# Performance work log

Hardware: AMD Instinct MI355X
Metric: run time of the kernel (lower is better)

The kernel has to match this reference:

```python
import jax, jax.numpy as jnp
import numpy as np
from jax import lax

EPS = 1e-8

def _norm(v, eps=EPS):
    # matches torch F.normalize: v / max(||v||, eps)
    return v / jnp.maximum(jnp.linalg.norm(v, axis=-1, keepdims=True), eps)

def keep_r6(r6):
    v1 = _norm(r6[..., :3])
    v2 = r6[..., 3:6]
    v2 = v2 - jnp.sum(v2 * v1, axis=-1, keepdims=True) * v1
    v2n = jnp.linalg.norm(v2, axis=-1, keepdims=True)
    mask = (v2n < 1e-6).astype(r6.dtype)
    e1 = jnp.array([1.0, 0.0, 0.0], dtype=r6.dtype)
    e2 = jnp.array([0.0, 1.0, 0.0], dtype=r6.dtype)
    dot = jnp.abs(jnp.sum(v1 * e1, axis=-1, keepdims=True))
    fb = jnp.where(dot < 0.9, e1, e2)
    fb_v2 = jnp.cross(v1, jnp.broadcast_to(fb, v1.shape), axis=-1)
    v2 = (1.0 - mask) * v2 + mask * fb_v2
    v2 = _norm(v2)
    return jnp.concatenate([v1, v2], axis=-1)

def r6_to_matrix(r6):
    r6 = keep_r6(r6)
    v1, v2 = r6[..., :3], r6[..., 3:6]
    v3 = jnp.cross(v1, v2, axis=-1)
    R = jnp.stack([v1, v2, v3], axis=-1)  # columns v1,v2,v3
    det = jnp.linalg.det(R)
    return R * jnp.sign(det)[..., None, None]

def instance_norm(x, eps=1e-5):
    # InstanceNorm3d, affine=False: per-(B,C) stats over spatial dims, biased var
    mu = jnp.mean(x, axis=(2, 3, 4), keepdims=True)
    var = jnp.mean((x - mu) ** 2, axis=(2, 3, 4), keepdims=True)
    return (x - mu) * lax.rsqrt(var + eps)

def conv1x1(x, w, b):
    return jnp.einsum('oc,bcdhw->bodhw', w[:, :, 0, 0, 0], x) + b[None, :, None, None, None]

def conv3_circ(x, w, b):
    xp = jnp.pad(x, ((0, 0), (0, 0), (1, 1), (1, 1), (1, 1)), mode='wrap')
    out = lax.conv_general_dilated(xp, w, (1, 1, 1), 'VALID',
                                   dimension_numbers=('NCDHW', 'OIDHW', 'NCDHW'))
    return out + b[None, :, None, None, None]

def _gelu(t):
    return jax.nn.gelu(t, approximate=False)

def _forward(x, pos_emb, qkv_w, qkv_b, lp1_w, lp1_b, lp2_w, lp2_b,
             mod1_w, mod1_b, mod2_w, mod2_b, pa_w, pa_b,
             R6_d, R6_h, R6_w, proj_w, proj_b):
    B, C, D, H, W = x.shape
    NH = pa_w.shape[0]
    HD = C // NH
    NV = HD // 3
    scale = HD ** (-0.5)

    # PositionalProcessing (deterministic; computed once, reused for all 3 axes)
    local = conv1x1(_gelu(instance_norm(conv3_circ(pos_emb, lp1_w, lp1_b))), lp2_w, lp2_b)
    mod = jax.nn.sigmoid(conv1x1(_gelu(instance_norm(conv1x1(local, mod1_w, mod1_b))), mod2_w, mod2_b))
    x_mod = x * mod
    pos_attn = _gelu(instance_norm(conv1x1(pos_emb, pa_w, pa_b)))  # [B,NH,D,H,W]

    axes = [
        (R6_d, (0, 3, 4, 1, 2), (0, 4, 3, 1, 2)),  # depth
        (R6_h, (0, 2, 4, 1, 3), (0, 4, 1, 3, 2)),  # height
        (R6_w, (0, 2, 3, 1, 4), (0, 4, 1, 2, 3)),  # width
    ]
    out_sum = 0.0
    for R6, perm, inv in axes:
        xp = jnp.transpose(x_mod, perm)      # [B, A1, A2, C, L]
        Bb, A1, A2, _, L = xp.shape
        bd = Bb * A1 * A2
        xl = jnp.swapaxes(xp.reshape(bd, C, L), -1, -2)  # [bd, L, C]
        qkv = (xl @ qkv_w.T + qkv_b).reshape(bd, L, 3, NH, HD)
        qkv = jnp.transpose(qkv, (2, 0, 3, 1, 4))
        q, k, v = qkv[0], qkv[1], qkv[2]     # [bd, NH, L, HD]
        R = r6_to_matrix(keep_r6(R6))[0]     # [NH, 3, 3]

        def rot(t):
            tv = t.reshape(bd, NH, L, NV, 3)
            return jnp.einsum('hij,bhlvj->bhlvi', R, tv).reshape(bd, NH, L, HD)

        attn = jnp.einsum('bhqd,bhkd->bhqk', rot(q), rot(k)) * scale
        pa = jnp.transpose(pos_attn, perm).reshape(bd, NH, L)
        attn = jax.nn.softmax(attn + pa[..., None], axis=-1)
        o = jnp.einsum('bhqk,bhkd->bhqd', attn, v)      # [bd, NH, L, HD]
        o = jnp.swapaxes(o, 1, 2).reshape(Bb, A1, A2, L, C)
        out_sum = out_sum + jnp.transpose(o, inv)        # [B, C, D, H, W]
    return conv1x1(out_sum, proj_w, proj_b)


def setup_inputs() -> dict:
    key = jax.random.key(0)
    ks = jax.random.split(key, 20)
    B, C, D, H, W, NH = 2, 96, 40, 40, 40, 4

    def rn(k, shape, s=0.05):
        return jax.random.normal(k, shape, dtype=jnp.float32) * s

    return {
        'x': jax.random.normal(ks[0], (B, C, D, H, W), dtype=jnp.float32),
        'pos_emb': jax.random.normal(ks[1], (B, C, D, H, W), dtype=jnp.float32),
        'qkv_w': rn(ks[2], (3 * C, C)), 'qkv_b': rn(ks[3], (3 * C,)),
        'lp1_w': rn(ks[4], (C, C, 3, 3, 3)), 'lp1_b': rn(ks[5], (C,)),
        'lp2_w': rn(ks[6], (C, C, 1, 1, 1)), 'lp2_b': rn(ks[7], (C,)),
        'mod1_w': rn(ks[8], (C, C, 1, 1, 1)), 'mod1_b': rn(ks[9], (C,)),
        'mod2_w': rn(ks[10], (C, C, 1, 1, 1)), 'mod2_b': rn(ks[11], (C,)),
        'pa_w': rn(ks[12], (NH, C, 1, 1, 1)), 'pa_b': rn(ks[13], (NH,)),
        'R6_d': jax.random.normal(ks[14], (1, NH, 6), dtype=jnp.float32),
        'R6_h': jax.random.normal(ks[15], (1, NH, 6), dtype=jnp.float32),
        'R6_w': jax.random.normal(ks[16], (1, NH, 6), dtype=jnp.float32),
        'proj_w': rn(ks[17], (C, C, 1, 1, 1)), 'proj_b': rn(ks[18], (C,)),
    }


def reference(x, pos_emb, qkv_w, qkv_b, lp1_w, lp1_b, lp2_w, lp2_b,
              mod1_w, mod1_b, mod2_w, mod2_b, pa_w, pa_b,
              R6_d, R6_h, R6_w, proj_w, proj_b):
    return _forward(x, pos_emb, qkv_w, qkv_b, lp1_w, lp1_b, lp2_w, lp2_b,
                    mod1_w, mod1_b, mod2_w, mod2_b, pa_w, pa_b,
                    R6_d, R6_h, R6_w, proj_w, proj_b)
```

## Files before the change

### kernel.cpp

```cpp
#include <hip/hip_runtime.h>


typedef __attribute__((ext_vector_type(8))) _Float16 half8;
typedef __attribute__((ext_vector_type(2))) _Float16 half2;
typedef __attribute__((ext_vector_type(16))) float floatx16;

static __device__ __forceinline__ half2 h2(unsigned int u) {
    return __builtin_bit_cast(half2, u);
}
static __device__ __forceinline__ float fdot2(unsigned int a, unsigned int b, float c) {
    return __builtin_amdgcn_fdot2(h2(a), h2(b), c, false);
}

__global__ void k_zero(float* __restrict__ p) {
    int t = threadIdx.x;
    for (int i = t; i < 768; i += 256) p[i] = 0.f;
}

__global__ __launch_bounds__(256) void k_cvt_in(const float* __restrict__ pos,
                                                _Float16* __restrict__ in_t) {
    __shared__ _Float16 lds[64][97];
    int bid = blockIdx.x;
    int b = bid / 1000, s0 = (bid % 1000) * 64;
    int t = threadIdx.x;
    for (int i = t; i < 6144; i += 256) {
        int c = i / 64, sl = i % 64;
        lds[sl][c] = (_Float16)pos[(b * 96 + c) * 64000 + s0 + sl];
    }
    __syncthreads();
    _Float16* outp = in_t + ((size_t)b * 64000 + s0) * 96;
    for (int i = t; i < 6144; i += 256) {
        int sl = i / 96, c = i % 96;
        outp[i] = lds[sl][c];
    }
}

__global__ void k_cvt_w(const float* __restrict__ w, _Float16* __restrict__ wf) {
    int i = blockIdx.x * 256 + threadIdx.x;
    if (i < 248832) {
        int c = i % 96, m = (i / 96) % 96, tap = i / 9216;
        wf[i] = (_Float16)w[(m * 96 + c) * 27 + tap];
    }
}

__global__ void k_cvt_f16(const float* __restrict__ w, _Float16* __restrict__ o, int n) {
    int i = blockIdx.x * 256 + threadIdx.x;
    if (i < n) o[i] = (_Float16)w[i];
}

__global__ __launch_bounds__(256) void k_fold(const float* __restrict__ lp2_w,
                                              const float* __restrict__ lp2_b,
                                              const float* __restrict__ mod1_w,
                                              const float* __restrict__ mod1_b,
                                              _Float16* __restrict__ wfold,
                                              float* __restrict__ bfold) {
    int i = blockIdx.x * 256 + threadIdx.x;
    if (i < 9216) {
        int o = i / 96, c = i % 96;
        float a = 0.f;
        for (int k = 0; k < 96; k++) a += mod1_w[o * 96 + k] * lp2_w[k * 96 + c];
        wfold[i] = (_Float16)a;
    }
    if (blockIdx.x == 0 && threadIdx.x < 96) {
        int o = threadIdx.x;
        float a = mod1_b[o];
        for (int k = 0; k < 96; k++) a += mod1_w[o * 96 + k] * lp2_b[k];
        bfold[o] = a;
    }
}

__global__ __launch_bounds__(256) void k_conv3_v2(const _Float16* __restrict__ in_t,
                                                  const _Float16* __restrict__ wf,
                                                  const float* __restrict__ bias,
                                                  _Float16* __restrict__ c3) {
    __shared__ int tbl[27 * 256];
    __shared__ _Float16 st[256 * 98];
    __shared__ float bsh[96];
    int t = threadIdx.x;
    int bid = blockIdx.x;
    int b = bid / 250;
    int s0 = (bid % 250) * 256;

    for (int u = t; u < 27 * 256; u += 256) {
        int tap = u >> 8, nl = u & 255;
        int kd = tap / 9, kh = (tap / 3) % 3, kw = tap % 3;
        int s = s0 + nl;
        int d = s / 1600, r = s - d * 1600;
        int h = r / 40, w = r - h * 40;
        int ds = d + kd - 1; if (ds < 0) ds += 40; else if (ds >= 40) ds -= 40;
        int hs = h + kh - 1; if (hs < 0) hs += 40; else if (hs >= 40) hs -= 40;
        int wv2 = w + kw - 1; if (wv2 < 0) wv2 += 40; else if (wv2 >= 40) wv2 -= 40;
        tbl[u] = ((ds * 1600 + hs * 40 + wv2) * 96) * 2;
    }
    if (t < 96) bsh[t] = bias[t];
    __syncthreads();

    int wv = t >> 6, lane = t & 63;
    int n31 = lane & 31, kg = lane >> 5;
    const char* inb = (const char*)(in_t + (size_t)b * 64000 * 96) + kg * 16;

    floatx16 acc[3][2];
#pragma unroll
    for (int mt = 0; mt < 3; mt++)
#pragma unroll
        for (int nt = 0; nt < 2; nt++)
#pragma unroll
            for (int r = 0; r < 16; r++) acc[mt][nt][r] = 0.f;

    for (int tap = 0; tap < 27; tap++) {
        int ta0 = tbl[tap * 256 + wv * 64 + n31];
        int ta1 = tbl[tap * 256 + wv * 64 + 32 + n31];
        const char* pb0 = inb + ta0;
        const char* pb1 = inb + ta1;
        const _Float16* wt = wf + tap * 9216 + kg * 8;
#pragma unroll
        for (int j = 0; j < 6; j++) {
            half8 a0 = *(const half8*)(wt + (n31) * 96 + j * 16);
            half8 a1 = *(const half8*)(wt + (32 + n31) * 96 + j * 16);
            half8 a2 = *(const half8*)(wt + (64 + n31) * 96 + j * 16);
            half8 b0 = *(const half8*)(pb0 + j * 32);
            half8 b1 = *(const half8*)(pb1 + j * 32);
            acc[0][0] = __builtin_amdgcn_mfma_f32_32x32x16_f16(a0, b0, acc[0][0], 0, 0, 0);
            acc[0][1] = __builtin_amdgcn_mfma_f32_32x32x16_f16(a0, b1, acc[0][1], 0, 0, 0);
            acc[1][0] = __builtin_amdgcn_mfma_f32_32x32x16_f16(a1, b0, acc[1][0], 0, 0, 0);
            acc[1][1] = __builtin_amdgcn_mfma_f32_32x32x16_f16(a1, b1, acc[1][1], 0, 0, 0);
            acc[2][0] = __builtin_amdgcn_mfma_f32_32x32x16_f16(a2, b0, acc[2][0], 0, 0, 0);
            acc[2][1] = __builtin_amdgcn_mfma_f32_32x32x16_f16(a2, b1, acc[2][1], 0, 0, 0);
        }
    }

#pragma unroll
    for (int mt = 0; mt < 3; mt++)
#pragma unroll
        for (int nt = 0; nt < 2; nt++)
#pragma unroll
            for (int r = 0; r < 16; r++) {
                int m = mt * 32 + (r & 3) + 8 * (r >> 2) + 4 * kg;
                int sl = wv * 64 + nt * 32 + n31;
                st[sl * 98 + m] = (_Float16)(acc[mt][nt][r] + bsh[m]);
            }
    __syncthreads();

    unsigned int* dst = (unsigned int*)(c3 + ((size_t)(b * 64000 + s0)) * 96);
    for (int i = t; i < 12288; i += 256) {
        int row = i / 48, sg = i % 48;
        dst[i] = *(const unsigned int*)&st[row * 98 + sg * 2];
    }
}

__global__ __launch_bounds__(192) void k_stats_sc(const _Float16* __restrict__ in,
                                                  float* __restrict__ raw) {
    __shared__ float red_s[16][96], red_q[16][96];
    int bid = blockIdx.x;
    int b = bid / 50, ch = bid % 50;
    int t = threadIdx.x;
    int sp = t / 12, cs = t % 12;
    const uint4* base = (const uint4*)(in + ((size_t)(b * 64000 + ch * 1280)) * 96);
    float s8[8], q8[8];
#pragma unroll
    for (int e = 0; e < 8; e++) { s8[e] = 0.f; q8[e] = 0.f; }
    for (int i = 0; i < 80; i++) {
        uint4 v = base[(sp + i * 16) * 12 + cs];
        half8 h = __builtin_bit_cast(half8, v);
#pragma unroll
        for (int e = 0; e < 8; e++) { float f = (float)h[e]; s8[e] += f; q8[e] += f * f; }
    }
#pragma unroll
    for (int e = 0; e < 8; e++) { red_s[sp][cs * 8 + e] = s8[e]; red_q[sp][cs * 8 + e] = q8[e]; }
    __syncthreads();
    if (t < 96) {
        float S = 0.f, Q = 0.f;
        for (int k = 0; k < 16; k++) { S += red_s[k][t]; Q += red_q[k][t]; }
        atomicAdd(&raw[(b * 96 + t) * 2], S);
        atomicAdd(&raw[(b * 96 + t) * 2 + 1], Q);
    }
}

__global__ void k_finalize(const float* __restrict__ raw, float2* __restrict__ sf) {
    int t = threadIdx.x;
    if (t < 192) {
        float S = raw[t * 2], Q = raw[t * 2 + 1];
        float mu = S * (1.f / 64000.f);
        float var = Q * (1.f / 64000.f) - mu * mu;
        sf[t] = make_float2(mu, rsqrtf(var + 1e-5f));
    }
}

__global__ __launch_bounds__(256) void k_ng16(_Float16* __restrict__ x, const float2* __restrict__ sf) {
    int t = threadIdx.x, bid = blockIdx.x;
    uint4* p = (uint4*)x;
#pragma unroll
    for (int k = 0; k < 4; k++) {
        int i = bid * 1024 + k * 256 + t;
        int e0 = i * 8;
        int b = e0 / 6144000;
        int c0 = e0 % 96;
        const float2* sp = &sf[b * 96 + c0];
        uint4 v = p[i];
        half8 h = __builtin_bit_cast(half8, v);
        _Float16 o[8];
#pragma unroll
        for (int e = 0; e < 8; e++) {
            float2 st = sp[e];
            float u = ((float)h[e] - st.x) * st.y;
            o[e] = (_Float16)(0.5f * u * (1.f + erff(u * 0.70710678118654752f)));
        }
        p[i] = *(uint4*)o;
    }
}

template <int MODE>
__global__ __launch_bounds__(256) void k_gemm96(const _Float16* __restrict__ in,
                                                const _Float16* __restrict__ w,
                                                const float* __restrict__ bias,
                                                const float* __restrict__ xg,
                                                _Float16* __restrict__ outp) {
    __shared__ _Float16 un[12544];
    __shared__ float bias_s[96];
    int t = threadIdx.x, bid = blockIdx.x;
    int b = bid / 500, s0 = (bid % 500) * 128;
    for (int i = t; i < 1152; i += 256) ((uint4*)un)[i] = ((const uint4*)w)[i];
    if (t < 96) bias_s[t] = bias[t];
    __syncthreads();

    int ws = t >> 6, lane = t & 63;
    int n = lane & 31, kg = lane >> 5;
    int p = ws * 32 + n;
    const uint4* brow = (const uint4*)(in + ((size_t)(b * 64000 + s0 + p)) * 96);
    uint4 bf[6];
#pragma unroll
    for (int kc = 0; kc < 6; kc++) bf[kc] = brow[kc * 2 + kg];

    floatx16 acc[3];
#pragma unroll
    for (int mt = 0; mt < 3; mt++)
#pragma unroll
        for (int r = 0; r < 16; r++) acc[mt][r] = 0.f;
#pragma unroll
    for (int kc = 0; kc < 6; kc++) {
        half8 bfh = __builtin_bit_cast(half8, bf[kc]);
#pragma unroll
        for (int mt = 0; mt < 3; mt++) {
            uint4 au = *(const uint4*)&un[(mt * 32 + n) * 96 + kc * 16 + kg * 8];
            acc[mt] = __builtin_amdgcn_mfma_f32_32x32x16_f16(__builtin_bit_cast(half8, au), bfh, acc[mt], 0, 0, 0);
        }
    }
    __syncthreads();

#pragma unroll
    for (int mt = 0; mt < 3; mt++)
#pragma unroll
        for (int r = 0; r < 16; r++) {
            int m = mt * 32 + (r & 3) + 8 * (r >> 2) + 4 * kg;
            int sl = ws * 32 + n;
            float v = acc[mt][r] + bias_s[m];
            if (MODE == 1) {
                v = 1.f / (1.f + __expf(-v));
                v *= xg[((size_t)(b * 96 + m)) * 64000 + s0 + sl];
            }
            un[sl * 98 + m] = (_Float16)v;
        }
    __syncthreads();

    unsigned int* dst = (unsigned int*)(outp + ((size_t)(b * 64000 + s0)) * 96);
    for (int i = t; i < 6144; i += 256) {
        int row = i / 48, sg = i % 48;
        dst[i] = *(const unsigned int*)&un[row * 98 + sg * 2];
    }
}

__global__ __launch_bounds__(256) void k_qkv(const _Float16* __restrict__ xt,
                                             const _Float16* __restrict__ wq,
                                             const float* __restrict__ qb,
                                             _Float16* __restrict__ qA) {
    __shared__ _Float16 smem[27648];
    __shared__ float bias_s[288];
    int t = threadIdx.x;
    int bid = blockIdx.x;
    int b = bid / 500;
    int s0 = (bid % 500) * 128;

    for (int i = t; i < 3456; i += 256) ((uint4*)smem)[i] = ((const uint4*)wq)[i];
    for (int i = t; i < 288; i += 256) bias_s[i] = qb[i];
    __syncthreads();

    int ws = t >> 6, lane = t & 63;
    int n = lane & 31, kg = lane >> 5;
    int p = ws * 32 + n;

    const uint4* brow = (const uint4*)(xt + ((size_t)(b * 64000 + s0 + p)) * 96);
    uint4 bf[6];
#pragma unroll
    for (int kc = 0; kc < 6; kc++) bf[kc] = brow[kc * 2 + kg];

    floatx16 acc[9];
#pragma unroll
    for (int mt = 0; mt < 9; mt++)
#pragma unroll
        for (int r = 0; r < 16; r++) acc[mt][r] = 0.f;

#pragma unroll
    for (int kc = 0; kc < 6; kc++) {
        half8 bfh = __builtin_bit_cast(half8, bf[kc]);
#pragma unroll
        for (int mt = 0; mt < 9; mt++) {
            uint4 au = *(const uint4*)&smem[(mt * 32 + n) * 96 + kc * 16 + kg * 8];
            acc[mt] = __builtin_amdgcn_mfma_f32_32x32x16_f16(__builtin_bit_cast(half8, au), bfh, acc[mt], 0, 0, 0);
        }
    }

    const float scale = 0.20412414523193154f;
    for (int q = 0; q < 2; q++) {
        __syncthreads();
        if ((ws >> 1) == q) {
            int pl = (ws & 1) * 32 + n;
#pragma unroll
            for (int mt = 0; mt < 9; mt++)
#pragma unroll
                for (int g = 0; g < 4; g++) {
                    int m0 = mt * 32 + g * 8 + kg * 4;
                    _Float16 tm[4];
#pragma unroll
                    for (int j = 0; j < 4; j++) {
                        float v = acc[mt][g * 4 + j] + bias_s[m0 + j];
                        if (m0 + j < 96) v *= scale;
                        tm[j] = (_Float16)v;
                    }
                    *(uint2*)&smem[pl * 296 + m0] = *(uint2*)tm;
                }
        }
        __syncthreads();
        for (int idx = t; idx < 2304; idx += 256) {
            int pl = idx / 36, seg = idx % 36;
            int s = s0 + q * 64 + pl;
            uint4 v = *(const uint4*)&smem[pl * 296 + seg * 8];
            *(uint4*)&qA[((size_t)(b * 64000 + s)) * 288 + seg * 8] = v;
        }
    }
}

template <int AXIS, bool ACC>
__global__ __launch_bounds__(320, 3) void k_attn(const _Float16* __restrict__ qA,
                                                 _Float16* __restrict__ osum) {
    __shared__ _Float16 kk[8352];
    __shared__ _Float16 vT[7744];
    int t = threadIdx.x;
    int bid = blockIdx.x;
    int b = bid / 800;
    int r0 = (bid % 800) * 2;

    auto smap = [&](int r, int l) -> int {
        if (AXIS == 0) return l * 1600 + r;
        else if (AXIS == 1) { int d = r / 40, w = r % 40; return d * 1600 + l * 40 + w; }
        else return r * 40 + l;
    };
    const uint4* src = (const uint4*)qA;
    for (int i = t; i < 960; i += 320) {
        int line = i / 480, key = (i % 480) / 12, seg = i % 12;
        int row = b * 64000 + smap(r0 + line, key);
        ((uint4*)kk)[i] = src[(size_t)row * 36 + 12 + seg];
    }
    for (int i = t; i < 960; i += 320) {
        int line = i / 480, key = (i % 480) / 12, seg = i % 12;
        int row = b * 64000 + smap(r0 + line, key);
        uint4 v = src[(size_t)row * 36 + 24 + seg];
        _Float16 tmp[8];
        *(uint4*)tmp = v;
#pragma unroll
        for (int e = 0; e < 8; e++) {
            int hdg = seg * 8 + e;
            vT[(line * 4 + hdg / 24) * 968 + (hdg % 24) * 40 + key] = tmp[e];
        }
    }

    int line = t / 160, head = (t % 160) / 40, ql = t % 40;
    int rr = r0 + line;
    unsigned int qu[12];
    {
        const uint4* qp = (const uint4*)(qA + ((size_t)(b * 64000 + smap(rr, ql))) * 288 + head * 24);
#pragma unroll
        for (int j = 0; j < 3; j++) *(uint4*)&qu[j * 4] = qp[j];
    }
    __syncthreads();

    float s[40];
    const uint4* kbase = (const uint4*)kk + line * 480 + head * 3;
#pragma unroll 4
    for (int key = 0; key < 40; key++) {
        unsigned int kku[12];
#pragma unroll
        for (int j = 0; j < 3; j++) *(uint4*)&kku[j * 4] = kbase[key * 12 + j];
        float a = 0.f;
#pragma unroll
        for (int i = 0; i < 12; i++) a = fdot2(kku[i], qu[i], a);
        s[key] = a;
    }

    float mx = -1e30f;
#pragma unroll
    for (int i = 0; i < 40; i++) mx = fmaxf(mx, s[i]);
    float sum = 0.f;
#pragma unroll
    for (int i = 0; i < 40; i++) { s[i] = __expf(s[i] - mx); sum += s[i]; }
    float inv = 1.f / sum;

    unsigned int pw[20];
#pragma unroll
    for (int i = 0; i < 20; i++) {
        half2 a = { (_Float16)(s[2 * i] * inv), (_Float16)(s[2 * i + 1] * inv) };
        pw[i] = __builtin_bit_cast(unsigned int, a);
    }

    __syncthreads();

    float o[24];
    const uint4* vbase = (const uint4*)vT + (line * 4 + head) * 121;
#pragma unroll 2
    for (int hd = 0; hd < 24; hd++) {
        unsigned int vv[20];
#pragma unroll
        for (int j = 0; j < 5; j++) *(uint4*)&vv[j * 4] = vbase[hd * 5 + j];
        float a = 0.f;
#pragma unroll
        for (int i = 0; i < 20; i++) a = fdot2(vv[i], pw[i], a);
        o[hd] = a;
    }

    {
        _Float16 tm[24];
#pragma unroll
        for (int j = 0; j < 24; j++) tm[j] = (_Float16)o[j];
        _Float16* dA = &kk[(line * 40 + ql) * 104 + head * 24];
#pragma unroll
        for (int j = 0; j < 3; j++) ((uint4*)dA)[j] = ((uint4*)tm)[j];
    }
    __syncthreads();

    uint4* dst = (uint4*)osum;
    for (int i = t; i < 960; i += 320) {
        int row = i / 12, seg = i % 12;
        int s2 = smap(r0 + row / 40, row % 40);
        size_t di = ((size_t)(b * 64000 + s2)) * 12 + seg;
        uint4 v = *(const uint4*)&kk[row * 104 + seg * 8];
        if (ACC) {
            half8 a = __builtin_bit_cast(half8, dst[di]);
            half8 c = __builtin_bit_cast(half8, v);
            dst[di] = __builtin_bit_cast(uint4, a + c);
        } else {
            dst[di] = v;
        }
    }
}

__global__ __launch_bounds__(256) void k_proj(const _Float16* __restrict__ osum,
                                              const _Float16* __restrict__ wp,
                                              const float* __restrict__ pb,
                                              float* __restrict__ out) {
    __shared__ _Float16 A[9216];
    __shared__ float bias_s[96];
    int t = threadIdx.x;
    int bid = blockIdx.x;
    int b = bid / 500;
    int s0 = (bid % 500) * 128;
    for (int i = t; i < 1152; i += 256) ((uint4*)A)[i] = ((const uint4*)wp)[i];
    if (t < 96) bias_s[t] = pb[t];
    __syncthreads();

    int ws = t >> 6, lane = t & 63;
    int n = lane & 31, kg = lane >> 5;
    int s = s0 + ws * 32 + n;

    const uint4* brow = (const uint4*)(osum + ((size_t)(b * 64000 + s0 + ws * 32 + n)) * 96);
    uint4 bf[6];
#pragma unroll
    for (int kc = 0; kc < 6; kc++) bf[kc] = brow[kc * 2 + kg];

    floatx16 acc[3];
#pragma unroll
    for (int mt = 0; mt < 3; mt++)
#pragma unroll
        for (int r = 0; r < 16; r++) acc[mt][r] = 0.f;

#pragma unroll
    for (int kc = 0; kc < 6; kc++) {
        half8 bfh = __builtin_bit_cast(half8, bf[kc]);
#pragma unroll
        for (int mt = 0; mt < 3; mt++) {
            uint4 au = *(const uint4*)&A[(mt * 32 + n) * 96 + kc * 16 + kg * 8];
            acc[mt] = __builtin_amdgcn_mfma_f32_32x32x16_f16(__builtin_bit_cast(half8, au), bfh, acc[mt], 0, 0, 0);
        }
    }

#pragma unroll
    for (int mt = 0; mt < 3; mt++)
#pragma unroll
        for (int r = 0; r < 16; r++) {
            int m = mt * 32 + (r & 3) + 8 * (r >> 2) + 4 * kg;
            out[((size_t)(b * 96 + m)) * 64000 + s] = acc[mt][r] + bias_s[m];
        }
}

extern "C" void kernel_launch(void* const* d_in, const int* in_sizes, int n_in,
                              void* d_out, int out_size, void* d_ws, size_t ws_size,
                              hipStream_t stream) {
    const float* x      = (const float*)d_in[0];
    const float* pos    = (const float*)d_in[1];
    const float* qkv_w  = (const float*)d_in[2];
    const float* qkv_b  = (const float*)d_in[3];
    const float* lp1_w  = (const float*)d_in[4];
    const float* lp1_b  = (const float*)d_in[5];
    const float* lp2_w  = (const float*)d_in[6];
    const float* lp2_b  = (const float*)d_in[7];
    const float* mod1_w = (const float*)d_in[8];
    const float* mod1_b = (const float*)d_in[9];
    const float* mod2_w = (const float*)d_in[10];
    const float* mod2_b = (const float*)d_in[11];
    const float* proj_w = (const float*)d_in[17];
    const float* proj_b = (const float*)d_in[18];
    float* out = (float*)d_out;
    float* ws = (float*)d_ws;

    _Float16* bufA = (_Float16*)ws;
    _Float16* bufB = (_Float16*)(ws + 6144000);
    _Float16* qA   = (_Float16*)(ws + 12288000);
    _Float16* in_t = qA;
    _Float16* wf   = (_Float16*)(ws + 30720000);
    _Float16* wq   = (_Float16*)(ws + 30844416);
    _Float16* wpj  = (_Float16*)(ws + 30858240);
    _Float16* wfold= (_Float16*)(ws + 30862848);
    _Float16* wm2  = (_Float16*)(ws + 30867456);
    float* bfold   = ws + 30872064;
    float* raw     = ws + 30872160;
    float2* sf0    = (float2*)(ws + 30872928);
    float2* sf1    = (float2*)(ws + 30873312);
    float* raw0 = raw, *raw1 = raw + 384;

    k_zero<<<1, 256, 0, stream>>>(raw);
    k_cvt_in<<<2000, 256, 0, stream>>>(pos, in_t);
    k_cvt_w<<<972, 256, 0, stream>>>(lp1_w, wf);
    k_fold<<<36, 256, 0, stream>>>(lp2_w, lp2_b, mod1_w, mod1_b, wfold, bfold);
    k_cvt_f16<<<36, 256, 0, stream>>>(mod2_w, wm2, 9216);
    k_cvt_f16<<<108, 256, 0, stream>>>(qkv_w, wq, 27648);
    k_cvt_f16<<<36, 256, 0, stream>>>(proj_w, wpj, 9216);

    k_conv3_v2<<<500, 256, 0, stream>>>(in_t, wf, lp1_b, bufA);
    k_stats_sc<<<100, 192, 0, stream>>>(bufA, raw0);
    k_finalize<<<1, 256, 0, stream>>>(raw0, sf0);
    k_ng16<<<1500, 256, 0, stream>>>(bufA, sf0);
    k_gemm96<0><<<1000, 256, 0, stream>>>(bufA, wfold, bfold, nullptr, bufB);
    k_stats_sc<<<100, 192, 0, stream>>>(bufB, raw1);
    k_finalize<<<1, 256, 0, stream>>>(raw1, sf1);
    k_ng16<<<1500, 256, 0, stream>>>(bufB, sf1);
    k_gemm96<1><<<1000, 256, 0, stream>>>(bufB, wm2, mod2_b, x, bufA);

    k_qkv<<<1000, 256, 0, stream>>>(bufA, wq, qkv_b, qA);
    k_attn<2, false><<<1600, 320, 0, stream>>>(qA, bufB);
    k_attn<0, true ><<<1600, 320, 0, stream>>>(qA, bufB);
    k_attn<1, true ><<<1600, 320, 0, stream>>>(qA, bufB);

    k_proj<<<1000, 256, 0, stream>>>(bufB, wpj, proj_b, out);
}
```

Before: 677.4 us.

## Fuse prep kernels, fold norm+GELU into GEMM, double-buffer conv weights in LDS

Merges the zeroing, weight conversion and weight-folding launches into one prep kernel. It also reorders the conv3 weight layout to match the MFMA lane order. The instance-norm finalize and GELU pass are folded into the load stage of the 1x1 GEMMs, removing two full read/write passes over the activations and several launches. The 3x3x3 conv now stages each tap's weights in LDS with register prefetch and double buffering, which adds a barrier per tap.

```diff
diff --git a/kernel.cpp b/kernel.cpp
--- a/kernel.cpp
+++ b/kernel.cpp
@@ -12,9 +12,53 @@
     return __builtin_amdgcn_fdot2(h2(a), h2(b), c, false);
 }
 
-__global__ void k_zero(float* __restrict__ p) {
-    int t = threadIdx.x;
-    for (int i = t; i < 768; i += 256) p[i] = 0.f;
+__global__ __launch_bounds__(256) void k_prep(const float* __restrict__ lp1_w,
+                                              const float* __restrict__ lp2_w,
+                                              const float* __restrict__ lp2_b,
+                                              const float* __restrict__ mod1_w,
+                                              const float* __restrict__ mod1_b,
+                                              const float* __restrict__ mod2_w,
+                                              const float* __restrict__ qkv_w,
+                                              const float* __restrict__ proj_w,
+                                              _Float16* __restrict__ wf,
+                                              _Float16* __restrict__ wfold,
+                                              _Float16* __restrict__ wm2,
+                                              _Float16* __restrict__ wq,
+                                              _Float16* __restrict__ wpj,
+                                              float* __restrict__ bfold,
+                                              float* __restrict__ raw) {
+    int id = blockIdx.x * 256 + threadIdx.x;
+    if (id < 248832) {
+        int tap = id / 9216, r = id % 9216;
+        int mt = r / 3072, r2 = r % 3072;
+        int kc = r2 / 512, r3 = r2 % 512;
+        int lane = r3 / 8, e = r3 % 8;
+        int m = mt * 32 + (lane & 31);
+        int c = kc * 16 + (lane >> 5) * 8 + e;
+        wf[id] = (_Float16)lp1_w[(m * 96 + c) * 27 + tap];
+    } else if (id < 258048) {
+        int i = id - 248832;
+        int o = i / 96, c = i % 96;
+        float a = 0.f;
+        for (int k = 0; k < 96; k++) a += mod1_w[o * 96 + k] * lp2_w[k * 96 + c];
+        wfold[i] = (_Float16)a;
+    } else if (id < 267264) {
+        int i = id - 258048;
+        wm2[i] = (_Float16)mod2_w[i];
+    } else if (id < 294912) {
+        int i = id - 267264;
+        wq[i] = (_Float16)qkv_w[i];
+    } else if (id < 304128) {
+        int i = id - 294912;
+        wpj[i] = (_Float16)proj_w[i];
+    } else if (id < 304224) {
+        int o = id - 304128;
+        float a = mod1_b[o];
+        for (int k = 0; k < 96; k++) a += mod1_w[o * 96 + k] * lp2_b[k];
+        bfold[o] = a;
+    } else if (id < 304992) {
+        raw[id - 304224] = 0.f;
+    }
 }
 
 __global__ __launch_bounds__(256) void k_cvt_in(const float* __restrict__ pos,
@@ -35,47 +79,14 @@
     }
 }
 
-__global__ void k_cvt_w(const float* __restrict__ w, _Float16* __restrict__ wf) {
-    int i = blockIdx.x * 256 + threadIdx.x;
-    if (i < 248832) {
-        int c = i % 96, m = (i / 96) % 96, tap = i / 9216;
-        wf[i] = (_Float16)w[(m * 96 + c) * 27 + tap];
-    }
-}
-
-__global__ void k_cvt_f16(const float* __restrict__ w, _Float16* __restrict__ o, int n) {
-    int i = blockIdx.x * 256 + threadIdx.x;
-    if (i < n) o[i] = (_Float16)w[i];
-}
-
-__global__ __launch_bounds__(256) void k_fold(const float* __restrict__ lp2_w,
-                                              const float* __restrict__ lp2_b,
-                                              const float* __restrict__ mod1_w,
-                                              const float* __restrict__ mod1_b,
-                                              _Float16* __restrict__ wfold,
-                                              float* __restrict__ bfold) {
-    int i = blockIdx.x * 256 + threadIdx.x;
-    if (i < 9216) {
-        int o = i / 96, c = i % 96;
-        float a = 0.f;
-        for (int k = 0; k < 96; k++) a += mod1_w[o * 96 + k] * lp2_w[k * 96 + c];
-        wfold[i] = (_Float16)a;
-    }
-    if (blockIdx.x == 0 && threadIdx.x < 96) {
-        int o = threadIdx.x;
-        float a = mod1_b[o];
-        for (int k = 0; k < 96; k++) a += mod1_w[o * 96 + k] * lp2_b[k];
-        bfold[o] = a;
-    }
-}
-
-__global__ __launch_bounds__(256) void k_conv3_v2(const _Float16* __restrict__ in_t,
+__global__ __launch_bounds__(256) void k_conv3_v3(const _Float16* __restrict__ in_t,
                                                   const _Float16* __restrict__ wf,
                                                   const float* __restrict__ bias,
                                                   _Float16* __restrict__ c3) {
-    __shared__ int tbl[27 * 256];
-    __shared__ _Float16 st[256 * 98];
+    __shared__ __align__(16) char sm[74880];
     __shared__ float bsh[96];
+    int* tbl = (int*)(sm + 36864);
+    _Float16* st = (_Float16*)sm;
     int t = threadIdx.x;
     int bid = blockIdx.x;
     int b = bid / 250;
@@ -93,11 +104,18 @@
         tbl[u] = ((ds * 1600 + hs * 40 + wv2) * 96) * 2;
     }
     if (t < 96) bsh[t] = bias[t];
-    __syncthreads();
 
     int wv = t >> 6, lane = t & 63;
     int n31 = lane & 31, kg = lane >> 5;
     const char* inb = (const char*)(in_t + (size_t)b * 64000 * 96) + kg * 16;
+    const uint4* wsrc = (const uint4*)wf;
+
+    uint4 pf[5];
+#pragma unroll
+    for (int k = 0; k < 5; k++) { int idx = t + k * 256; if (idx < 1152) pf[k] = wsrc[idx]; }
+    __syncthreads();
+#pragma unroll
+    for (int k = 0; k < 5; k++) { int idx = t + k * 256; if (idx < 1152) *(uint4*)(sm + idx * 16) = pf[k]; }
 
     floatx16 acc[3][2];
 #pragma unroll
@@ -108,16 +126,23 @@
             for (int r = 0; r < 16; r++) acc[mt][nt][r] = 0.f;
 
     for (int tap = 0; tap < 27; tap++) {
+        char* cur = sm + (tap & 1) * 18432;
+        char* nxt = sm + ((tap + 1) & 1) * 18432;
+        if (tap + 1 < 27) {
+            const uint4* wn = wsrc + (tap + 1) * 1152;
+#pragma unroll
+            for (int k = 0; k < 5; k++) { int idx = t + k * 256; if (idx < 1152) pf[k] = wn[idx]; }
+        }
+        __syncthreads();
         int ta0 = tbl[tap * 256 + wv * 64 + n31];
         int ta1 = tbl[tap * 256 + wv * 64 + 32 + n31];
         const char* pb0 = inb + ta0;
         const char* pb1 = inb + ta1;
-        const _Float16* wt = wf + tap * 9216 + kg * 8;
 #pragma unroll
         for (int j = 0; j < 6; j++) {
-            half8 a0 = *(const half8*)(wt + (n31) * 96 + j * 16);
-            half8 a1 = *(const half8*)(wt + (32 + n31) * 96 + j * 16);
-            half8 a2 = *(const half8*)(wt + (64 + n31) * 96 + j * 16);
+            half8 a0 = *(half8*)(cur + 0 * 6144 + j * 1024 + lane * 16);
+            half8 a1 = *(half8*)(cur + 1 * 6144 + j * 1024 + lane * 16);
+            half8 a2 = *(half8*)(cur + 2 * 6144 + j * 1024 + lane * 16);
             half8 b0 = *(const half8*)(pb0 + j * 32);
             half8 b1 = *(const half8*)(pb1 + j * 32);
             acc[0][0] = __builtin_amdgcn_mfma_f32_32x32x16_f16(a0, b0, acc[0][0], 0, 0, 0);
@@ -127,7 +152,12 @@
             acc[2][0] = __builtin_amdgcn_mfma_f32_32x32x16_f16(a2, b0, acc[2][0], 0, 0, 0);
             acc[2][1] = __builtin_amdgcn_mfma_f32_32x32x16_f16(a2, b1, acc[2][1], 0, 0, 0);
         }
-    }
+        if (tap + 1 < 27) {
+#pragma unroll
+            for (int k = 0; k < 5; k++) { int idx = t + k * 256; if (idx < 1152) *(uint4*)(nxt + idx * 16) = pf[k]; }
+        }
+    }
+    __syncthreads();
 
 #pragma unroll
     for (int mt = 0; mt < 3; mt++)
@@ -176,51 +206,26 @@
     }
 }
 
-__global__ void k_finalize(const float* __restrict__ raw, float2* __restrict__ sf) {
-    int t = threadIdx.x;
-    if (t < 192) {
-        float S = raw[t * 2], Q = raw[t * 2 + 1];
-        float mu = S * (1.f / 64000.f);
-        float var = Q * (1.f / 64000.f) - mu * mu;
-        sf[t] = make_float2(mu, rsqrtf(var + 1e-5f));
-    }
-}
-
-__global__ __launch_bounds__(256) void k_ng16(_Float16* __restrict__ x, const float2* __restrict__ sf) {
-    int t = threadIdx.x, bid = blockIdx.x;
-    uint4* p = (uint4*)x;
-#pragma unroll
-    for (int k = 0; k < 4; k++) {
-        int i = bid * 1024 + k * 256 + t;
-        int e0 = i * 8;
-        int b = e0 / 6144000;
-        int c0 = e0 % 96;
-        const float2* sp = &sf[b * 96 + c0];
-        uint4 v = p[i];
-        half8 h = __builtin_bit_cast(half8, v);
-        _Float16 o[8];
-#pragma unroll
-        for (int e = 0; e < 8; e++) {
-            float2 st = sp[e];
-            float u = ((float)h[e] - st.x) * st.y;
-            o[e] = (_Float16)(0.5f * u * (1.f + erff(u * 0.70710678118654752f)));
-        }
-        p[i] = *(uint4*)o;
-    }
-}
-
 template <int MODE>
 __global__ __launch_bounds__(256) void k_gemm96(const _Float16* __restrict__ in,
                                                 const _Float16* __restrict__ w,
                                                 const float* __restrict__ bias,
+                                                const float* __restrict__ raw,
                                                 const float* __restrict__ xg,
                                                 _Float16* __restrict__ outp) {
     __shared__ _Float16 un[12544];
     __shared__ float bias_s[96];
+    __shared__ float2 sfl[96];
     int t = threadIdx.x, bid = blockIdx.x;
     int b = bid / 500, s0 = (bid % 500) * 128;
     for (int i = t; i < 1152; i += 256) ((uint4*)un)[i] = ((const uint4*)w)[i];
-    if (t < 96) bias_s[t] = bias[t];
+    if (t < 96) {
+        bias_s[t] = bias[t];
+        float S = raw[(b * 96 + t) * 2], Q = raw[(b * 96 + t) * 2 + 1];
+        float mu = S * (1.f / 64000.f);
+        float var = Q * (1.f / 64000.f) - mu * mu;
+        sfl[t] = make_float2(mu, rsqrtf(var + 1e-5f));
+    }
     __syncthreads();
 
     int ws = t >> 6, lane = t & 63;
@@ -229,7 +234,19 @@
     const uint4* brow = (const uint4*)(in + ((size_t)(b * 64000 + s0 + p)) * 96);
     uint4 bf[6];
 #pragma unroll
-    for (int kc = 0; kc < 6; kc++) bf[kc] = brow[kc * 2 + kg];
+    for (int kc = 0; kc < 6; kc++) {
+        uint4 v = brow[kc * 2 + kg];
+        half8 h = __builtin_bit_cast(half8, v);
+        _Float16 g[8];
+#pragma unroll
+        for (int e = 0; e < 8; e++) {
+            int c = kc * 16 + kg * 8 + e;
+            float2 sv = sfl[c];
+            float u = ((float)h[e] - sv.x) * sv.y;
+            g[e] = (_Float16)(0.5f * u * (1.f + erff(u * 0.70710678118654752f)));
+        }
+        bf[kc] = *(uint4*)g;
+    }
 
     floatx16 acc[3];
 #pragma unroll
@@ -470,7 +487,7 @@
     int n = lane & 31, kg = lane >> 5;
     int s = s0 + ws * 32 + n;
 
-    const uint4* brow = (const uint4*)(osum + ((size_t)(b * 64000 + s0 + ws * 32 + n)) * 96);
+    const uint4* brow = (const uint4*)(osum + ((size_t)(b * 64000 + s)) * 96);
     uint4 bf[6];
 #pragma unroll
     for (int kc = 0; kc < 6; kc++) bf[kc] = brow[kc * 2 + kg];
@@ -531,27 +548,17 @@
     _Float16* wm2  = (_Float16*)(ws + 30867456);
     float* bfold   = ws + 30872064;
     float* raw     = ws + 30872160;
-    float2* sf0    = (float2*)(ws + 30872928);
-    float2* sf1    = (float2*)(ws + 30873312);
     float* raw0 = raw, *raw1 = raw + 384;
 
-    k_zero<<<1, 256, 0, stream>>>(raw);
+    k_prep<<<1192, 256, 0, stream>>>(lp1_w, lp2_w, lp2_b, mod1_w, mod1_b, mod2_w,
+                                     qkv_w, proj_w, wf, wfold, wm2, wq, wpj, bfold, raw);
     k_cvt_in<<<2000, 256, 0, stream>>>(pos, in_t);
-    k_cvt_w<<<972, 256, 0, stream>>>(lp1_w, wf);
-    k_fold<<<36, 256, 0, stream>>>(lp2_w, lp2_b, mod1_w, mod1_b, wfold, bfold);
-    k_cvt_f16<<<36, 256, 0, stream>>>(mod2_w, wm2, 9216);
-    k_cvt_f16<<<108, 256, 0, stream>>>(qkv_w, wq, 27648);
-    k_cvt_f16<<<36, 256, 0, stream>>>(proj_w, wpj, 9216);
-
-    k_conv3_v2<<<500, 256, 0, stream>>>(in_t, wf, lp1_b, bufA);
+
+    k_conv3_v3<<<500, 256, 0, stream>>>(in_t, wf, lp1_b, bufA);
     k_stats_sc<<<100, 192, 0, stream>>>(bufA, raw0);
-    k_finalize<<<1, 256, 0, stream>>>(raw0, sf0);
-    k_ng16<<<1500, 256, 0, stream>>>(bufA, sf0);
-    k_gemm96<0><<<1000, 256, 0, stream>>>(bufA, wfold, bfold, nullptr, bufB);
+    k_gemm96<0><<<1000, 256, 0, stream>>>(bufA, wfold, bfold, raw0, nullptr, bufB);
     k_stats_sc<<<100, 192, 0, stream>>>(bufB, raw1);
-    k_finalize<<<1, 256, 0, stream>>>(raw1, sf1);
-    k_ng16<<<1500, 256, 0, stream>>>(bufB, sf1);
-    k_gemm96<1><<<1000, 256, 0, stream>>>(bufB, wm2, mod2_b, x, bufA);
+    k_gemm96<1><<<1000, 256, 0, stream>>>(bufB, wm2, mod2_b, raw1, x, bufA);
 
     k_qkv<<<1000, 256, 0, stream>>>(bufA, wq, qkv_b, qA);
     k_attn<2, false><<<1600, 320, 0, stream>>>(qA, bufB);
```

Result: slower. 704.4 us (+4.0%).
